# Optimization experiments

Hardware: AMD Instinct MI355X
Metric: run time of the kernel (lower is better)

## Reference

```python
import jax, jax.numpy as jnp
import numpy as np
from jax import lax

B, N_ENT, D_ENT = 64, 512, 256
C_SCAT, C_MAP, W = 32, 18, 64
N_RES = 4


def conv2d(x, w, stride, pad):
    return lax.conv_general_dilated(x, w, (stride, stride), [(pad, pad), (pad, pad)],
                                    dimension_numbers=('NCHW', 'OIHW', 'NCHW'))


def batchnorm(x, g, b, eps=1e-5):
    # training-mode BN (batch statistics), matching nn.BatchNorm2d default train()
    mu = x.mean((0, 2, 3), keepdims=True)
    var = x.var((0, 2, 3), keepdims=True)
    return g[None, :, None, None] * (x - mu) * lax.rsqrt(var + eps) + b[None, :, None, None]


def setup_inputs() -> dict:
    key = jax.random.key(0)
    ks = jax.random.split(key, 24)
    s = 0.05
    inp = {
        'x': jax.random.uniform(ks[0], (B, C_MAP, W, W), jnp.float32),
        'entity_embeddings': jax.random.normal(ks[1], (B, N_ENT, D_ENT), jnp.float32),
        'entity_x_y': jax.random.randint(ks[2], (B, N_ENT, 16), 0, 2, jnp.int32),
        'conv1_w': jax.random.normal(ks[3], (C_SCAT, D_ENT), jnp.float32) * s,
        'project_w': jax.random.normal(ks[4], (32, C_SCAT + C_MAP, 1, 1), jnp.float32) * s,
        'project_b': jnp.zeros((32,), jnp.float32),
        'ds1_w': jax.random.normal(ks[5], (64, 32, 4, 4), jnp.float32) * s,
        'ds1_b': jnp.zeros((64,), jnp.float32),
        'ds2_w': jax.random.normal(ks[6], (128, 64, 4, 4), jnp.float32) * s,
        'ds2_b': jnp.zeros((128,), jnp.float32),
        'ds3_w': jax.random.normal(ks[7], (128, 128, 4, 4), jnp.float32) * s,
        'ds3_b': jnp.zeros((128,), jnp.float32),
        'res_conv1_w': jax.random.normal(ks[8], (N_RES, 128, 128, 3, 3), jnp.float32) * s,
        'res_bn1_g': jnp.ones((N_RES, 128), jnp.float32),
        'res_bn1_b': jnp.zeros((N_RES, 128), jnp.float32),
        'res_conv2_w': jax.random.normal(ks[9], (N_RES, 128, 128, 3, 3), jnp.float32) * s,
        'res_bn2_g': jnp.ones((N_RES, 128), jnp.float32),
        'res_bn2_b': jnp.zeros((N_RES, 128), jnp.float32),
        'fc_w': jax.random.normal(ks[10], (256, 8 * 8 * 128), jnp.float32) * s,
        'fc_b': jnp.zeros((256,), jnp.float32),
    }
    return inp


def _scatter(entity_embeddings, entity_x_y, conv1_w):
    # reduced = relu(Conv1d(256->32, k=1)) on entity dim
    reduced = jax.nn.relu(jnp.einsum('bnd,cd->bnc', entity_embeddings, conv1_w))  # [B,N,32]
    bits = entity_x_y
    pow2 = (2 ** jnp.arange(7, -1, -1)).astype(jnp.int32)
    xv = (bits[..., :8] * pow2).sum(-1) // 4   # [B,N] in 0..63
    yv = (bits[..., 8:] * pow2).sum(-1) // 4
    valid = (bits[..., 0] != -1000000000)
    reduced = reduced * valid[..., None].astype(reduced.dtype)
    b_idx = jnp.arange(entity_embeddings.shape[0], dtype=jnp.int32)[:, None]
    flat = (b_idx * (W * W) + yv * W + xv).reshape(-1)
    scat = jax.ops.segment_sum(reduced.reshape(-1, C_SCAT), flat, num_segments=entity_embeddings.shape[0] * W * W)
    return scat.reshape(-1, W, W, C_SCAT).transpose(0, 3, 1, 2)  # [B,32,W,W]


def reference(x, entity_embeddings, entity_x_y, conv1_w, project_w, project_b,
              ds1_w, ds1_b, ds2_w, ds2_b, ds3_w, ds3_b,
              res_conv1_w, res_bn1_g, res_bn1_b, res_conv2_w, res_bn2_g, res_bn2_b,
              fc_w, fc_b):
    scatter_map = _scatter(entity_embeddings, entity_x_y, conv1_w)
    h = jnp.concatenate([scatter_map, x], axis=1)  # [B,50,64,64]
    h = jax.nn.relu(conv2d(h, project_w, 1, 0) + project_b[None, :, None, None])
    h = jax.nn.relu(conv2d(h, ds1_w, 2, 1) + ds1_b[None, :, None, None])   # [B,64,32,32]
    h = jax.nn.relu(conv2d(h, ds2_w, 2, 1) + ds2_b[None, :, None, None])   # [B,128,16,16]
    h = jax.nn.relu(conv2d(h, ds3_w, 2, 1) + ds3_b[None, :, None, None])   # [B,128,8,8]
    map_skip = h
    for i in range(N_RES):
        identity = h
        o = batchnorm(conv2d(h, res_conv1_w[i], 1, 1), res_bn1_g[i], res_bn1_b[i])
        o = jax.nn.relu(o)
        o = batchnorm(conv2d(o, res_conv2_w[i], 1, 1), res_bn2_g[i], res_bn2_b[i])
        h = jax.nn.relu(o + identity)
        map_skip = map_skip + h
    flat = h.reshape(h.shape[0], -1)
    embedded_spatial = jax.nn.relu(flat @ fc_w.T + fc_b)
    return (map_skip, embedded_spatial)
```

## Files before the change

kernel.cpp:

```cpp
#include <hip/hip_runtime.h>
#include <hip/hip_bf16.h>

typedef __attribute__((ext_vector_type(8))) short bf16x8;
typedef __attribute__((ext_vector_type(4))) short bf16x4;
typedef __attribute__((ext_vector_type(4))) float f32x4;

__device__ __forceinline__ short f2bs(float v) {
  __hip_bfloat16 h = __float2bfloat16(v);
  return *reinterpret_cast<short*>(&h);
}

__global__ __launch_bounds__(256) void k_wall(
    const float* __restrict__ rc1w, const float* __restrict__ rc2w,
    const float* __restrict__ d1w, const float* __restrict__ d2w,
    const float* __restrict__ d3w, const float* __restrict__ fcw,
    const float* __restrict__ c1w, const float* __restrict__ pw,
    short* __restrict__ wTr1, short* __restrict__ wTr2, short* __restrict__ wTds1,
    short* __restrict__ wTds2, short* __restrict__ wTds3, short* __restrict__ wfcbf,
    short* __restrict__ wsc, short* __restrict__ wproj) {
  __shared__ float ld[128 * 65];
  const int bx = blockIdx.x;
  const int tid = threadIdx.x;
  if (bx < 4608) {
    const float* src = (bx < 2304) ? rc1w : rc2w;
    short* dst = (bx < 2304) ? wTr1 : wTr2;
    const int i = (bx % 2304) * 256 + tid;
    if (i < 589824) {
      const int layer = i / 147456;
      const int rem = i % 147456;
      const int tap = rem / 16384;
      const int r2 = rem & 16383;
      const int co = r2 >> 7, ci = r2 & 127;
      dst[i] = f2bs(src[(((size_t)layer * 16384 + co * 128 + ci) * 9) + tap]);
    }
  } else if (bx < 6272) {
    int CIN, n, base;
    const float* src;
    short* dst;
    if (bx < 4736) { CIN = 32; n = 32768; base = 4608; src = d1w; dst = wTds1; }
    else if (bx < 5248) { CIN = 64; n = 131072; base = 4736; src = d2w; dst = wTds2; }
    else { CIN = 128; n = 262144; base = 5248; src = d3w; dst = wTds3; }
    const int i = (bx - base) * 256 + tid;
    if (i < n) {
      const int COCI = n / 16;
      const int tap = i / COCI;
      const int rem = i % COCI;
      dst[i] = f2bs(src[(size_t)rem * 16 + tap]);
    }
  } else if (bx < 6528) {
    const int j = bx - 6272;
    const float* sp = fcw + (size_t)j * 8192;
    for (int i = tid; i < 8192; i += 256) {
      const int co = i >> 6, pix = i & 63;
      ld[co * 65 + pix] = sp[i];
    }
    __syncthreads();
    short* dp = wfcbf + (size_t)j * 8192;
    for (int i = tid; i < 8192; i += 256) {
      const int pix = i >> 7, co = i & 127;
      dp[i] = f2bs(ld[co * 65 + pix]);
    }
  } else if (bx < 6560) {
    const int i = (bx - 6528) * 256 + tid;
    if (i < 8192) wsc[i] = f2bs(c1w[i]);
  } else {
    const int i = (bx - 6560) * 256 + tid;
    if (i < 2048) {
      const int co = i >> 6, k = i & 63;
      wproj[i] = (k < 50) ? f2bs(pw[co * 50 + k]) : (short)0;
    }
  }
}

__global__ __launch_bounds__(256) void k_scatmfma(const float* __restrict__ emb,
                                                  const int* __restrict__ xy,
                                                  const short* __restrict__ wsc,
                                                  float* __restrict__ scat_pm) {
  constexpr int CIP = 264;
  __shared__ short abf[64 * CIP];
  __shared__ int flat[64];
  const int tid = threadIdx.x;
  const int e0 = blockIdx.x * 64;
  const float4* eg = (const float4*)(emb + (size_t)e0 * 256);
  for (int i = tid; i < 4096; i += 256) {
    const int e = i >> 6, k4 = i & 63;
    const float4 v = eg[(size_t)e * 64 + k4];
    bf16x4 o;
    o[0] = f2bs(v.x); o[1] = f2bs(v.y); o[2] = f2bs(v.z); o[3] = f2bs(v.w);
    *(bf16x4*)(&abf[e * CIP + k4 * 4]) = o;
  }
  if (tid < 64) {
    const int* bp = xy + (size_t)(e0 + tid) * 16;
    int xv = 0, yv = 0;
#pragma unroll
    for (int j = 0; j < 8; ++j) xv = (xv << 1) | bp[j];
#pragma unroll
    for (int j = 8; j < 16; ++j) yv = (yv << 1) | bp[j];
    flat[tid] = (bp[0] != -1000000000)
                    ? (((e0 + tid) >> 9) * 4096 + ((yv >> 2) << 6) + (xv >> 2))
                    : -1;
  }
  __syncthreads();
  const int wq = __builtin_amdgcn_readfirstlane(tid >> 6);
  const int lane = tid & 63;
  const int l15 = lane & 15, quad = lane >> 4;
  f32x4 acc[2];
  acc[0] = (f32x4){0.f, 0.f, 0.f, 0.f};
  acc[1] = (f32x4){0.f, 0.f, 0.f, 0.f};
  const short* arow = &abf[(wq * 16 + l15) * CIP + quad * 8];
  const short* w0 = wsc + (size_t)l15 * 256 + quad * 8;
  const short* w1 = wsc + (size_t)(16 + l15) * 256 + quad * 8;
#pragma unroll
  for (int kk = 0; kk < 8; ++kk) {
    bf16x8 a = *(const bf16x8*)(arow + kk * 32);
    acc[0] = __builtin_amdgcn_mfma_f32_16x16x32_bf16(a, *(const bf16x8*)(w0 + kk * 32), acc[0], 0, 0, 0);
    acc[1] = __builtin_amdgcn_mfma_f32_16x16x32_bf16(a, *(const bf16x8*)(w1 + kk * 32), acc[1], 0, 0, 0);
  }
#pragma unroll
  for (int nt = 0; nt < 2; ++nt)
#pragma unroll
    for (int r = 0; r < 4; ++r) {
      const int e = wq * 16 + quad * 4 + r;
      const float v = acc[nt][r];
      const int f = flat[e];
      if (f >= 0 && v > 0.f)
        atomicAdd(&scat_pm[(size_t)f * 32 + nt * 16 + l15], v);
    }
}

__global__ __launch_bounds__(256) void k_projmfma(const float* __restrict__ scat_pm,
                                                  const float* __restrict__ xin,
                                                  const short* __restrict__ wproj,
                                                  const float* __restrict__ pb,
                                                  short* __restrict__ h0pm) {
  constexpr int PK = 72;
  __shared__ short abf[128 * PK];
  const int tid = threadIdx.x;
  const int b = blockIdx.x >> 5;
  const int yx0 = (blockIdx.x & 31) << 7;
  const float4* sg = (const float4*)(scat_pm + ((size_t)(b * 4096 + yx0)) * 32);
  for (int i = tid; i < 1024; i += 256) {
    const int p = i >> 3, c4 = i & 7;
    const float4 v = sg[(size_t)p * 8 + c4];
    bf16x4 o;
    o[0] = f2bs(v.x); o[1] = f2bs(v.y); o[2] = f2bs(v.z); o[3] = f2bs(v.w);
    *(bf16x4*)(&abf[p * PK + c4 * 4]) = o;
  }
  for (int i = tid; i < 2304; i += 256) {
    const int run = i >> 7, p = i & 127;
    abf[p * PK + 32 + run] = f2bs(xin[(size_t)(b * 18 + run) * 4096 + yx0 + p]);
  }
  for (int i = tid; i < 2048; i += 256) {
    const int p = i >> 4, k = 50 + (i & 15);
    abf[p * PK + k] = 0;
  }
  __syncthreads();
  const int wq = __builtin_amdgcn_readfirstlane(tid >> 6);
  const int lane = tid & 63;
  const int l15 = lane & 15, quad = lane >> 4;
  f32x4 acc[2][2];
#pragma unroll
  for (int t = 0; t < 2; ++t)
#pragma unroll
    for (int n = 0; n < 2; ++n) acc[t][n] = (f32x4){0.f, 0.f, 0.f, 0.f};
  const short* wb0 = wproj + (size_t)l15 * 64 + quad * 8;
  const short* wb1 = wproj + (size_t)(16 + l15) * 64 + quad * 8;
#pragma unroll
  for (int kk = 0; kk < 2; ++kk) {
    const bf16x8 b0 = *(const bf16x8*)(wb0 + kk * 32);
    const bf16x8 b1 = *(const bf16x8*)(wb1 + kk * 32);
#pragma unroll
    for (int t = 0; t < 2; ++t) {
      const int pix = (wq * 2 + t) * 16 + l15;
      bf16x8 a = *(const bf16x8*)(&abf[pix * PK + quad * 8 + kk * 32]);
      acc[t][0] = __builtin_amdgcn_mfma_f32_16x16x32_bf16(a, b0, acc[t][0], 0, 0, 0);
      acc[t][1] = __builtin_amdgcn_mfma_f32_16x16x32_bf16(a, b1, acc[t][1], 0, 0, 0);
    }
  }
#pragma unroll
  for (int t = 0; t < 2; ++t)
#pragma unroll
    for (int n = 0; n < 2; ++n) {
      const int co = n * 16 + l15;
      const float bv = pb[co];
#pragma unroll
      for (int r = 0; r < 4; ++r) {
        const int pix = (wq * 2 + t) * 16 + quad * 4 + r;
        float v = acc[t][n][r] + bv;
        v = v > 0.f ? v : 0.f;
        h0pm[((size_t)(b * 4096 + yx0 + pix)) * 32 + co] = f2bs(v);
      }
    }
}

template <int CIN, int COUT, int HIN, int ROWSO, int COSPLIT, int MT, int NT, int OUTMODE>
__global__ __launch_bounds__(256) void k_ds2(const short* __restrict__ inpm,
                                             const short* __restrict__ wT,
                                             const float* __restrict__ bias,
                                             short* __restrict__ outbf,
                                             float* __restrict__ outf,
                                             float* __restrict__ msf) {
  constexpr int HOUT = HIN / 2;
  constexpr int ROWS = 2 * ROWSO + 2;
  constexpr int COLS = HIN + 2;
  constexpr int CHUNKS = CIN / 8;
  constexpr int KK = CIN / 32;
  constexpr int CIPAD = CIN + 8;
  constexpr int NHO = HOUT / ROWSO;
  __shared__ short lin[ROWS * COLS * CIPAD];
  const int tid = threadIdx.x;
  int bx = blockIdx.x;
  const int co_blk = (COSPLIT > 1) ? (bx % COSPLIT) : 0;
  if (COSPLIT > 1) bx /= COSPLIT;
  const int hoblk = bx % NHO;
  const int b = bx / NHO;
  for (int i = tid; i < ROWS * COLS * CHUNKS; i += 256) {
    const int ch = i % CHUNKS;
    const int pixv = i / CHUNKS;
    const int r = pixv / COLS, c = pixv % COLS;
    const int hi = 2 * ROWSO * hoblk - 1 + r;
    const int wc = c - 1;
    bf16x8 v = (bf16x8)(short)0;
    if (hi >= 0 && hi < HIN && wc >= 0 && wc < HIN)
      v = *(const bf16x8*)(inpm + ((size_t)(b * HIN + hi) * HIN + wc) * CIN + ch * 8);
    *(bf16x8*)(&lin[(r * COLS + c) * CIPAD + ch * 8]) = v;
  }
  __syncthreads();
  const int wq = __builtin_amdgcn_readfirstlane(tid >> 6);
  const int lane = tid & 63;
  const int l15 = lane & 15, quad = lane >> 4;
  const int mtile = (MT > 1) ? (wq % MT) : 0;
  const int cogrp = wq / MT;
  const int cobase = co_blk * (COUT / COSPLIT) + cogrp * (NT * 16);
  const int p = mtile * 16 + l15;
  const int dr = p / HOUT;
  const int col = p % HOUT;
  f32x4 acc[NT];
#pragma unroll
  for (int n = 0; n < NT; ++n) acc[n] = (f32x4){0.f, 0.f, 0.f, 0.f};
  const short* wrow = wT + (size_t)(cobase + l15) * CIN + quad * 8;
  for (int ky = 0; ky < 4; ++ky) {
    for (int kx = 0; kx < 4; ++kx) {
      const short* arow = &lin[((2 * dr + ky) * COLS + 2 * col + kx) * CIPAD + quad * 8];
      const short* wt = wrow + (size_t)(ky * 4 + kx) * COUT * CIN;
#pragma unroll
      for (int kk = 0; kk < KK; ++kk) {
        bf16x8 a = *(const bf16x8*)(arow + kk * 32);
#pragma unroll
        for (int n = 0; n < NT; ++n) {
          bf16x8 bf = *(const bf16x8*)(wt + n * 16 * CIN + kk * 32);
          acc[n] = __builtin_amdgcn_mfma_f32_16x16x32_bf16(a, bf, acc[n], 0, 0, 0);
        }
      }
    }
  }
#pragma unroll
  for (int n = 0; n < NT; ++n) {
    const int co = cobase + n * 16 + l15;
    const float bv = bias[co];
#pragma unroll
    for (int r = 0; r < 4; ++r) {
      const int pp = mtile * 16 + quad * 4 + r;
      const int dr2 = pp / HOUT;
      const int c2 = pp % HOUT;
      const int ho = hoblk * ROWSO + dr2;
      float v = acc[n][r] + bv;
      v = v > 0.f ? v : 0.f;
      const size_t o = ((size_t)b * HOUT * HOUT + ho * HOUT + c2) * COUT + co;
      outbf[o] = f2bs(v);
      if (OUTMODE == 1) {
        outf[o] = v;
        msf[o] = v;
      }
    }
  }
}

template <int BNIN>
__global__ __launch_bounds__(256) void k_resmfma(const short* __restrict__ hbfin,
                                                 const float* __restrict__ fin,
                                                 const float* __restrict__ statsIn,
                                                 const float* __restrict__ gIn,
                                                 const float* __restrict__ bIn,
                                                 const short* __restrict__ wT,
                                                 float* __restrict__ outpm,
                                                 float* __restrict__ statsOut) {
  constexpr int CIPAD = 136;
  __shared__ short lin[100 * CIPAD];
  __shared__ float bnsc[128], bnsh[128];
  const int tid = threadIdx.x;
  const int b = blockIdx.x >> 3;
  const int cobase = (blockIdx.x & 7) << 4;
  if (BNIN == 1) {
    if (tid < 128) {
      const float mu = statsIn[tid] * (1.f / 4096.f);
      const float var = statsIn[128 + tid] * (1.f / 4096.f) - mu * mu;
      const float sc = gIn[tid] * rsqrtf(var + 1e-5f);
      bnsc[tid] = sc;
      bnsh[tid] = bIn[tid] - mu * sc;
    }
    __syncthreads();
  }
  if (BNIN == 0) {
    const short* hb = hbfin + ((size_t)b << 13);
    for (int i = tid; i < 1600; i += 256) {
      const int pixel = i >> 4, ch = i & 15;
      const int r = pixel / 10, c = pixel % 10;
      bf16x8 v = (bf16x8)(short)0;
      if (r >= 1 && r <= 8 && c >= 1 && c <= 8)
        v = *(const bf16x8*)(hb + (((r - 1) << 3) + (c - 1)) * 128 + ch * 8);
      *(bf16x8*)(&lin[pixel * CIPAD + ch * 8]) = v;
    }
  } else {
    const float* fb = fin + ((size_t)b << 13);
    for (int i = tid; i < 3200; i += 256) {
      const int pixel = i >> 5, c4 = i & 31;
      const int r = pixel / 10, c = pixel % 10;
      bf16x4 o = (bf16x4)(short)0;
      if (r >= 1 && r <= 8 && c >= 1 && c <= 8) {
        const float4 x = *(const float4*)(fb + (size_t)(((r - 1) << 3) + (c - 1)) * 128 + c4 * 4);
        const float xv[4] = {x.x, x.y, x.z, x.w};
#pragma unroll
        for (int k = 0; k < 4; ++k) {
          const int ci = c4 * 4 + k;
          const float v = xv[k] * bnsc[ci] + bnsh[ci];
          o[k] = f2bs(v > 0.f ? v : 0.f);
        }
      }
      *(bf16x4*)(&lin[pixel * CIPAD + c4 * 4]) = o;
    }
  }
  __syncthreads();
  const int wq = __builtin_amdgcn_readfirstlane(tid >> 6);
  const int lane = tid & 63;
  const int l15 = lane & 15, quad = lane >> 4;
  const int p = wq * 16 + l15;
  const int py = p >> 3, px = p & 7;
  f32x4 acc = (f32x4){0.f, 0.f, 0.f, 0.f};
  const short* wrow = wT + (size_t)(cobase + l15) * 128 + quad * 8;
  for (int t = 0; t < 9; ++t) {
    const int ky = t / 3, kx = t % 3;
    const short* arow = &lin[((py + ky) * 10 + px + kx) * CIPAD + quad * 8];
    const short* wt = wrow + (size_t)t * 16384;
#pragma unroll
    for (int kk = 0; kk < 4; ++kk) {
      bf16x8 a = *(const bf16x8*)(arow + kk * 32);
      bf16x8 bf = *(const bf16x8*)(wt + kk * 32);
      acc = __builtin_amdgcn_mfma_f32_16x16x32_bf16(a, bf, acc, 0, 0, 0);
    }
  }
  float* ob = outpm + ((size_t)b << 13);
  const int co = cobase + l15;
  float s = 0.f, q = 0.f;
#pragma unroll
  for (int r = 0; r < 4; ++r) {
    const float v = acc[r];
    ob[(size_t)(wq * 16 + quad * 4 + r) * 128 + co] = v;
    s += v;
    q += v * v;
  }
  s += __shfl_down(s, 32); q += __shfl_down(q, 32);
  s += __shfl_down(s, 16); q += __shfl_down(q, 16);
  if (lane < 16) {
    atomicAdd(&statsOut[co], s);
    atomicAdd(&statsOut[128 + co], q);
  }
}

__global__ __launch_bounds__(256) void k_bnadd(const float* __restrict__ inpm,
                                               const float* __restrict__ stats,
                                               const float* __restrict__ g,
                                               const float* __restrict__ bb,
                                               const float* __restrict__ identpm,
                                               float* __restrict__ houtpm,
                                               short* __restrict__ houtbf,
                                               float* __restrict__ mspm) {
  const int idx = blockIdx.x * 256 + threadIdx.x;
  const int co = idx & 127;
  const float mu = stats[co] * (1.f / 4096.f);
  const float var = stats[128 + co] * (1.f / 4096.f) - mu * mu;
  float v = g[co] * (inpm[idx] - mu) * rsqrtf(var + 1e-5f) + bb[co];
  v += identpm[idx];
  v = v > 0.f ? v : 0.f;
  houtpm[idx] = v;
  houtbf[idx] = f2bs(v);
  mspm[idx] += v;
}

__global__ __launch_bounds__(256) void k_mstrans(const float* __restrict__ mspm,
                                                 float* __restrict__ out0) {
  __shared__ float t[64 * 132];
  const int b = blockIdx.x;
  const int tid = threadIdx.x;
  const float* sp = mspm + ((size_t)b << 13);
  for (int i = tid; i < 8192; i += 256) {
    const int pix = i >> 7, co = i & 127;
    t[pix * 132 + co] = sp[i];
  }
  __syncthreads();
  float* dp = out0 + ((size_t)b << 13);
  for (int i = tid; i < 8192; i += 256) {
    const int co = i >> 6, pix = i & 63;
    dp[i] = t[pix * 132 + co];
  }
}

__global__ __launch_bounds__(256) void k_fcmfma(const short* __restrict__ hbf,
                                                const short* __restrict__ wbf,
                                                float* __restrict__ part) {
  const int nb = blockIdx.x & 3;
  const int kb = blockIdx.x >> 2;
  const int wq = __builtin_amdgcn_readfirstlane((int)(threadIdx.x >> 6));
  const int lane = threadIdx.x & 63;
  const int l15 = lane & 15, quad = lane >> 4;
  const int k0 = kb * 256 + quad * 8;
  const short* wp = wbf + (size_t)(nb * 64 + wq * 16 + l15) * 8192 + k0;
  const short* hp = hbf + (size_t)l15 * 8192 + k0;
  f32x4 acc[4];
#pragma unroll
  for (int m = 0; m < 4; ++m) acc[m] = (f32x4){0.f, 0.f, 0.f, 0.f};
  for (int ks = 0; ks < 8; ++ks) {
    bf16x8 bfr = *(const bf16x8*)(wp + ks * 32);
#pragma unroll
    for (int m = 0; m < 4; ++m) {
      bf16x8 a = *(const bf16x8*)(hp + (size_t)m * 16 * 8192 + ks * 32);
      acc[m] = __builtin_amdgcn_mfma_f32_16x16x32_bf16(a, bfr, acc[m], 0, 0, 0);
    }
  }
#pragma unroll
  for (int m = 0; m < 4; ++m)
#pragma unroll
    for (int r = 0; r < 4; ++r) {
      const int b = m * 16 + quad * 4 + r;
      part[((size_t)kb * 64 + b) * 256 + nb * 64 + wq * 16 + l15] = acc[m][r];
    }
}

__global__ __launch_bounds__(256) void k_fcred(const float* __restrict__ part,
                                               const float* __restrict__ bias,
                                               float* __restrict__ out1) {
  const int idx = blockIdx.x * 256 + threadIdx.x;
  const int j = idx & 255;
  float s = 0.f;
#pragma unroll 8
  for (int kb = 0; kb < 32; ++kb) s += part[(size_t)kb * 16384 + idx];
  const float v = s + bias[j];
  out1[idx] = v > 0.f ? v : 0.f;
}

extern "C" void kernel_launch(void* const* d_in, const int* in_sizes, int n_in,
                              void* d_out, int out_size, void* d_ws, size_t ws_size,
                              hipStream_t stream) {
  const float* xin = (const float*)d_in[0];
  const float* emb = (const float*)d_in[1];
  const int* xy = (const int*)d_in[2];
  const float* c1w = (const float*)d_in[3];
  const float* pw = (const float*)d_in[4];
  const float* pb = (const float*)d_in[5];
  const float* d1w = (const float*)d_in[6];
  const float* d1b = (const float*)d_in[7];
  const float* d2w = (const float*)d_in[8];
  const float* d2b = (const float*)d_in[9];
  const float* d3w = (const float*)d_in[10];
  const float* d3b = (const float*)d_in[11];
  const float* rc1w = (const float*)d_in[12];
  const float* rbn1g = (const float*)d_in[13];
  const float* rbn1b = (const float*)d_in[14];
  const float* rc2w = (const float*)d_in[15];
  const float* rbn2g = (const float*)d_in[16];
  const float* rbn2b = (const float*)d_in[17];
  const float* fcw = (const float*)d_in[18];
  const float* fcb = (const float*)d_in[19];

  float* out0 = (float*)d_out;
  float* out1 = out0 + 524288;

  float* F = (float*)d_ws;
  float* scat = F + 0;
  float* h1pm_f = F + 0;
  float* h2pm_f = F + 2097152;
  float* hApm = F + 3145728;
  float* hBpm = F + 3670016;
  float* tmppm = F + 4194304;
  float* tmp2pm = F + 4718592;
  float* mspm = F + 5242880;
  short* pmbfA = (short*)(F + 5767168);
  short* pmbfB = (short*)(F + 6029312);
  float* stats = F + 6291456;
  float* fcpart = F + 6293504;
  short* h0pm = (short*)(F + 8388608);
  short* wfcbf = (short*)(F + 12582912);
  short* wTr1 = (short*)(F + 13631488);
  short* wTr2 = wTr1 + 589824;
  short* wTds1 = wTr2 + 589824;
  short* wTds2 = wTds1 + 32768;
  short* wTds3 = wTds2 + 131072;
  short* wsc = wTds3 + 262144;
  short* wproj = wsc + 8192;

  hipMemsetAsync(scat, 0, 8388608 * sizeof(float), stream);
  k_wall<<<6568, 256, 0, stream>>>(rc1w, rc2w, d1w, d2w, d3w, fcw, c1w, pw,
                                   wTr1, wTr2, wTds1, wTds2, wTds3, wfcbf, wsc, wproj);
  k_scatmfma<<<512, 256, 0, stream>>>(emb, xy, wsc, scat);
  k_projmfma<<<2048, 256, 0, stream>>>(scat, xin, wproj, pb, h0pm);
  hipMemsetAsync(stats, 0, 2048 * sizeof(float), stream);
  short* h1pm = (short*)h1pm_f;
  short* h2pm = (short*)h2pm_f;
  k_ds2<32, 64, 64, 2, 1, 4, 4, 0><<<1024, 256, 0, stream>>>(h0pm, wTds1, d1b, h1pm, hApm, mspm);
  k_ds2<64, 128, 32, 1, 1, 1, 2, 0><<<1024, 256, 0, stream>>>(h1pm, wTds2, d2b, h2pm, hApm, mspm);
  k_ds2<128, 128, 16, 2, 2, 1, 1, 1><<<512, 256, 0, stream>>>(h2pm, wTds3, d3b, pmbfA, hApm, mspm);

  float* cur = hApm;  float* nxt = hBpm;
  short* curbf = pmbfA; short* nxtbf = pmbfB;
  for (int i = 0; i < 4; ++i) {
    float* sA = stats + i * 512;
    float* sB = stats + i * 512 + 256;
    k_resmfma<0><<<512, 256, 0, stream>>>(curbf, nullptr, nullptr, nullptr, nullptr,
                                          wTr1 + (size_t)i * 147456, tmppm, sA);
    k_resmfma<1><<<512, 256, 0, stream>>>(nullptr, tmppm, sA, rbn1g + i * 128, rbn1b + i * 128,
                                          wTr2 + (size_t)i * 147456, tmp2pm, sB);
    k_bnadd<<<2048, 256, 0, stream>>>(tmp2pm, sB, rbn2g + i * 128, rbn2b + i * 128, cur, nxt,
                                      nxtbf, mspm);
    float* sw = cur; cur = nxt; nxt = sw;
    short* swb = curbf; curbf = nxtbf; nxtbf = swb;
  }
  k_mstrans<<<64, 256, 0, stream>>>(mspm, out0);
  k_fcmfma<<<128, 256, 0, stream>>>(curbf, wfcbf, fcpart);
  k_fcred<<<64, 256, 0, stream>>>(fcpart, fcb, out1);
}
```

Before: 405.4 us.

## Fuse BN-add residual epilogue into next conv prologue and fold memsets into weight kernel

Removes the separate k_bnadd kernel by applying BN2+identity+ReLU inside the next residual conv's input staging (a new BNIN=2 variant); only the cobase==0 block writes the fp32 h and map_skip updates. The final block's BN-add is merged with the map_skip transpose into a new k_bnfinal kernel. The scatter-buffer and stats memsets are folded into the weight-conversion kernel as extra blocks. This saves kernel launches and a full activation round-trip per residual block, at the cost of each of the 8 co-blocks recomputing the BN-add for the whole image.

```diff
diff --git a/kernel.cpp b/kernel.cpp
--- a/kernel.cpp
+++ b/kernel.cpp
@@ -17,14 +17,17 @@
     const float* __restrict__ c1w, const float* __restrict__ pw,
     short* __restrict__ wTr1, short* __restrict__ wTr2, short* __restrict__ wTds1,
     short* __restrict__ wTds2, short* __restrict__ wTds3, short* __restrict__ wfcbf,
-    short* __restrict__ wsc, short* __restrict__ wproj) {
+    short* __restrict__ wsc, short* __restrict__ wproj,
+    float* __restrict__ scat, float* __restrict__ stats) {
   __shared__ float ld[128 * 65];
   const int bx = blockIdx.x;
   const int tid = threadIdx.x;
-  if (bx < 4608) {
-    const float* src = (bx < 2304) ? rc1w : rc2w;
-    short* dst = (bx < 2304) ? wTr1 : wTr2;
-    const int i = (bx % 2304) * 256 + tid;
+  if (bx < 8192) {
+    ((float4*)scat)[(size_t)bx * 256 + tid] = make_float4(0.f, 0.f, 0.f, 0.f);
+  } else if (bx < 12800) {
+    const float* src = (bx < 10496) ? rc1w : rc2w;
+    short* dst = (bx < 10496) ? wTr1 : wTr2;
+    const int i = ((bx - 8192) % 2304) * 256 + tid;
     if (i < 589824) {
       const int layer = i / 147456;
       const int rem = i % 147456;
@@ -33,13 +36,13 @@
       const int co = r2 >> 7, ci = r2 & 127;
       dst[i] = f2bs(src[(((size_t)layer * 16384 + co * 128 + ci) * 9) + tap]);
     }
-  } else if (bx < 6272) {
-    int CIN, n, base;
+  } else if (bx < 14464) {
+    int n, base;
     const float* src;
     short* dst;
-    if (bx < 4736) { CIN = 32; n = 32768; base = 4608; src = d1w; dst = wTds1; }
-    else if (bx < 5248) { CIN = 64; n = 131072; base = 4736; src = d2w; dst = wTds2; }
-    else { CIN = 128; n = 262144; base = 5248; src = d3w; dst = wTds3; }
+    if (bx < 12928) { n = 32768; base = 12800; src = d1w; dst = wTds1; }
+    else if (bx < 13440) { n = 131072; base = 12928; src = d2w; dst = wTds2; }
+    else { n = 262144; base = 13440; src = d3w; dst = wTds3; }
     const int i = (bx - base) * 256 + tid;
     if (i < n) {
       const int COCI = n / 16;
@@ -47,8 +50,8 @@
       const int rem = i % COCI;
       dst[i] = f2bs(src[(size_t)rem * 16 + tap]);
     }
-  } else if (bx < 6528) {
-    const int j = bx - 6272;
+  } else if (bx < 14720) {
+    const int j = bx - 14464;
     const float* sp = fcw + (size_t)j * 8192;
     for (int i = tid; i < 8192; i += 256) {
       const int co = i >> 6, pix = i & 63;
@@ -60,15 +63,17 @@
       const int pix = i >> 7, co = i & 127;
       dp[i] = f2bs(ld[co * 65 + pix]);
     }
-  } else if (bx < 6560) {
-    const int i = (bx - 6528) * 256 + tid;
+  } else if (bx < 14752) {
+    const int i = (bx - 14720) * 256 + tid;
     if (i < 8192) wsc[i] = f2bs(c1w[i]);
-  } else {
-    const int i = (bx - 6560) * 256 + tid;
+  } else if (bx < 14760) {
+    const int i = (bx - 14752) * 256 + tid;
     if (i < 2048) {
       const int co = i >> 6, k = i & 63;
       wproj[i] = (k < 50) ? f2bs(pw[co * 50 + k]) : (short)0;
     }
+  } else {
+    for (int i = tid; i < 2048; i += 256) stats[i] = 0.f;
   }
 }
 
@@ -282,6 +287,9 @@
                                                  const float* __restrict__ statsIn,
                                                  const float* __restrict__ gIn,
                                                  const float* __restrict__ bIn,
+                                                 const float* __restrict__ identpm,
+                                                 float* __restrict__ houtpm,
+                                                 float* __restrict__ mspm,
                                                  const short* __restrict__ wT,
                                                  float* __restrict__ outpm,
                                                  float* __restrict__ statsOut) {
@@ -291,7 +299,7 @@
   const int tid = threadIdx.x;
   const int b = blockIdx.x >> 3;
   const int cobase = (blockIdx.x & 7) << 4;
-  if (BNIN == 1) {
+  if (BNIN >= 1) {
     if (tid < 128) {
       const float mu = statsIn[tid] * (1.f / 4096.f);
       const float var = statsIn[128 + tid] * (1.f / 4096.f) - mu * mu;
@@ -311,7 +319,7 @@
         v = *(const bf16x8*)(hb + (((r - 1) << 3) + (c - 1)) * 128 + ch * 8);
       *(bf16x8*)(&lin[pixel * CIPAD + ch * 8]) = v;
     }
-  } else {
+  } else if (BNIN == 1) {
     const float* fb = fin + ((size_t)b << 13);
     for (int i = tid; i < 3200; i += 256) {
       const int pixel = i >> 5, c4 = i & 31;
@@ -325,6 +333,39 @@
           const int ci = c4 * 4 + k;
           const float v = xv[k] * bnsc[ci] + bnsh[ci];
           o[k] = f2bs(v > 0.f ? v : 0.f);
+        }
+      }
+      *(bf16x4*)(&lin[pixel * CIPAD + c4 * 4]) = o;
+    }
+  } else {
+    const float* fb = fin + ((size_t)b << 13);
+    const float* ib = identpm + ((size_t)b << 13);
+    float* hb = houtpm + ((size_t)b << 13);
+    float* mb = mspm + ((size_t)b << 13);
+    const bool wr = (cobase == 0);
+    for (int i = tid; i < 3200; i += 256) {
+      const int pixel = i >> 5, c4 = i & 31;
+      const int r = pixel / 10, c = pixel % 10;
+      bf16x4 o = (bf16x4)(short)0;
+      if (r >= 1 && r <= 8 && c >= 1 && c <= 8) {
+        const size_t gi = (size_t)(((r - 1) << 3) + (c - 1)) * 128 + c4 * 4;
+        const float4 x = *(const float4*)(fb + gi);
+        const float4 idv = *(const float4*)(ib + gi);
+        const float xv[4] = {x.x, x.y, x.z, x.w};
+        const float iv[4] = {idv.x, idv.y, idv.z, idv.w};
+        float vv[4];
+#pragma unroll
+        for (int k = 0; k < 4; ++k) {
+          const int ci = c4 * 4 + k;
+          float v = xv[k] * bnsc[ci] + bnsh[ci] + iv[k];
+          v = v > 0.f ? v : 0.f;
+          vv[k] = v;
+          o[k] = f2bs(v);
+        }
+        if (wr) {
+          *(float4*)(hb + gi) = make_float4(vv[0], vv[1], vv[2], vv[3]);
+          const float4 m = *(const float4*)(mb + gi);
+          *(float4*)(mb + gi) = make_float4(m.x + vv[0], m.y + vv[1], m.z + vv[2], m.w + vv[3]);
         }
       }
       *(bf16x4*)(&lin[pixel * CIPAD + c4 * 4]) = o;
@@ -367,38 +408,36 @@
   }
 }
 
-__global__ __launch_bounds__(256) void k_bnadd(const float* __restrict__ inpm,
-                                               const float* __restrict__ stats,
-                                               const float* __restrict__ g,
-                                               const float* __restrict__ bb,
-                                               const float* __restrict__ identpm,
-                                               float* __restrict__ houtpm,
-                                               short* __restrict__ houtbf,
-                                               float* __restrict__ mspm) {
-  const int idx = blockIdx.x * 256 + threadIdx.x;
-  const int co = idx & 127;
-  const float mu = stats[co] * (1.f / 4096.f);
-  const float var = stats[128 + co] * (1.f / 4096.f) - mu * mu;
-  float v = g[co] * (inpm[idx] - mu) * rsqrtf(var + 1e-5f) + bb[co];
-  v += identpm[idx];
-  v = v > 0.f ? v : 0.f;
-  houtpm[idx] = v;
-  houtbf[idx] = f2bs(v);
-  mspm[idx] += v;
-}
-
-__global__ __launch_bounds__(256) void k_mstrans(const float* __restrict__ mspm,
-                                                 float* __restrict__ out0) {
+__global__ __launch_bounds__(256) void k_bnfinal(const float* __restrict__ tmp2pm,
+                                                 const float* __restrict__ stats,
+                                                 const float* __restrict__ g,
+                                                 const float* __restrict__ bb,
+                                                 const float* __restrict__ identpm,
+                                                 const float* __restrict__ mspm,
+                                                 float* __restrict__ out0,
+                                                 short* __restrict__ hbf) {
   __shared__ float t[64 * 132];
+  __shared__ float bnsc[128], bnsh[128];
   const int b = blockIdx.x;
   const int tid = threadIdx.x;
-  const float* sp = mspm + ((size_t)b << 13);
+  if (tid < 128) {
+    const float mu = stats[tid] * (1.f / 4096.f);
+    const float var = stats[128 + tid] * (1.f / 4096.f) - mu * mu;
+    const float sc = g[tid] * rsqrtf(var + 1e-5f);
+    bnsc[tid] = sc;
+    bnsh[tid] = bb[tid] - mu * sc;
+  }
+  __syncthreads();
+  const size_t base = (size_t)b << 13;
   for (int i = tid; i < 8192; i += 256) {
-    const int pix = i >> 7, co = i & 127;
-    t[pix * 132 + co] = sp[i];
+    const int co = i & 127, pix = i >> 7;
+    float v = tmp2pm[base + i] * bnsc[co] + bnsh[co] + identpm[base + i];
+    v = v > 0.f ? v : 0.f;
+    hbf[base + i] = f2bs(v);
+    t[pix * 132 + co] = mspm[base + i] + v;
   }
   __syncthreads();
-  float* dp = out0 + ((size_t)b << 13);
+  float* dp = out0 + base;
   for (int i = tid; i < 8192; i += 256) {
     const int co = i >> 6, pix = i & 63;
     dp[i] = t[pix * 132 + co];
@@ -485,7 +524,7 @@
   float* tmp2pm = F + 4718592;
   float* mspm = F + 5242880;
   short* pmbfA = (short*)(F + 5767168);
-  short* pmbfB = (short*)(F + 6029312);
+  short* hfinbf = (short*)(F + 6029312);
   float* stats = F + 6291456;
   float* fcpart = F + 6293504;
   short* h0pm = (short*)(F + 8388608);
@@ -498,33 +537,39 @@
   short* wsc = wTds3 + 262144;
   short* wproj = wsc + 8192;
 
-  hipMemsetAsync(scat, 0, 8388608 * sizeof(float), stream);
-  k_wall<<<6568, 256, 0, stream>>>(rc1w, rc2w, d1w, d2w, d3w, fcw, c1w, pw,
-                                   wTr1, wTr2, wTds1, wTds2, wTds3, wfcbf, wsc, wproj);
+  k_wall<<<14761, 256, 0, stream>>>(rc1w, rc2w, d1w, d2w, d3w, fcw, c1w, pw,
+                                    wTr1, wTr2, wTds1, wTds2, wTds3, wfcbf, wsc, wproj,
+                                    scat, stats);
   k_scatmfma<<<512, 256, 0, stream>>>(emb, xy, wsc, scat);
   k_projmfma<<<2048, 256, 0, stream>>>(scat, xin, wproj, pb, h0pm);
-  hipMemsetAsync(stats, 0, 2048 * sizeof(float), stream);
   short* h1pm = (short*)h1pm_f;
   short* h2pm = (short*)h2pm_f;
   k_ds2<32, 64, 64, 2, 1, 4, 4, 0><<<1024, 256, 0, stream>>>(h0pm, wTds1, d1b, h1pm, hApm, mspm);
   k_ds2<64, 128, 32, 1, 1, 1, 2, 0><<<1024, 256, 0, stream>>>(h1pm, wTds2, d2b, h2pm, hApm, mspm);
   k_ds2<128, 128, 16, 2, 2, 1, 1, 1><<<512, 256, 0, stream>>>(h2pm, wTds3, d3b, pmbfA, hApm, mspm);
 
-  float* cur = hApm;  float* nxt = hBpm;
-  short* curbf = pmbfA; short* nxtbf = pmbfB;
+  float* ident = hApm;
+  float* identN = hBpm;
   for (int i = 0; i < 4; ++i) {
     float* sA = stats + i * 512;
     float* sB = stats + i * 512 + 256;
-    k_resmfma<0><<<512, 256, 0, stream>>>(curbf, nullptr, nullptr, nullptr, nullptr,
-                                          wTr1 + (size_t)i * 147456, tmppm, sA);
+    if (i == 0) {
+      k_resmfma<0><<<512, 256, 0, stream>>>(pmbfA, nullptr, nullptr, nullptr, nullptr,
+                                            nullptr, nullptr, nullptr,
+                                            wTr1, tmppm, sA);
+    } else {
+      float* sBp = stats + (i - 1) * 512 + 256;
+      k_resmfma<2><<<512, 256, 0, stream>>>(nullptr, tmp2pm, sBp, rbn2g + (i - 1) * 128,
+                                            rbn2b + (i - 1) * 128, ident, identN, mspm,
+                                            wTr1 + (size_t)i * 147456, tmppm, sA);
+      float* sw = ident; ident = identN; identN = sw;
+    }
     k_resmfma<1><<<512, 256, 0, stream>>>(nullptr, tmppm, sA, rbn1g + i * 128, rbn1b + i * 128,
+                                          nullptr, nullptr, nullptr,
                                           wTr2 + (size_t)i * 147456, tmp2pm, sB);
-    k_bnadd<<<2048, 256, 0, stream>>>(tmp2pm, sB, rbn2g + i * 128, rbn2b + i * 128, cur, nxt,
-                                      nxtbf, mspm);
-    float* sw = cur; cur = nxt; nxt = sw;
-    short* swb = curbf; curbf = nxtbf; nxtbf = swb;
-  }
-  k_mstrans<<<64, 256, 0, stream>>>(mspm, out0);
-  k_fcmfma<<<128, 256, 0, stream>>>(curbf, wfcbf, fcpart);
+  }
+  k_bnfinal<<<64, 256, 0, stream>>>(tmp2pm, stats + 3 * 512 + 256, rbn2g + 384, rbn2b + 384,
+                                    ident, mspm, out0, hfinbf);
+  k_fcmfma<<<128, 256, 0, stream>>>(hfinbf, wfcbf, fcpart);
   k_fcred<<<64, 256, 0, stream>>>(fcpart, fcb, out1);
 }
```

New measurement: 412.2 us. About the same (+1.7%).
